# Kernel optimization log

Hardware: AMD Instinct MI355X
Metric: run time of the kernel (lower is better)

## Reference

```python
import jax, jax.numpy as jnp
import numpy as np

B, T, D = 2, 2048, 1024
N_HEADS = 16
HEAD_DIM = D // N_HEADS
HIDDEN = 4 * D
LN_EPS = 1e-6  # flax LayerNorm default


def apply_rotary_pos_emb(x, positions):
    # x: (B, T, H, head_dim); positions: (T,)
    head_dim = x.shape[-1]
    inv_freq = 1.0 / 10000 ** (jnp.arange(0, head_dim, 2).astype(jnp.float32) / head_dim)
    freqs = jnp.outer(positions.astype(jnp.float32), inv_freq)  # (T, head_dim//2)
    cos_emb = jnp.cos(freqs)[None, :, None, :]
    sin_emb = jnp.sin(freqs)[None, :, None, :]
    x1 = x[..., : head_dim // 2]
    x2 = x[..., head_dim // 2 :]
    return jnp.concatenate([x1 * cos_emb - x2 * sin_emb,
                            x1 * sin_emb + x2 * cos_emb], axis=-1)


def layernorm(x, scale, bias):
    mu = jnp.mean(x, axis=-1, keepdims=True)
    var = jnp.mean(jnp.square(x - mu), axis=-1, keepdims=True)
    return (x - mu) * jax.lax.rsqrt(var + LN_EPS) * scale + bias


def setup_inputs() -> dict:
    key = jax.random.key(0)
    ks = jax.random.split(key, 8)
    lecun = lambda k, shape: jax.random.normal(k, shape, jnp.float32) * (1.0 / np.sqrt(shape[0]))
    x = jax.random.normal(ks[0], (B, T, D), jnp.float32)
    positions = jnp.arange(T, dtype=jnp.int32)
    mask = jnp.tril(jnp.ones((T, T), dtype=bool))[None, None]  # causal (1,1,T,T)
    return {
        "x": x,
        "positions": positions,
        "mask": mask,
        "ln1_scale": jnp.ones((D,), jnp.float32),
        "ln1_bias": jnp.zeros((D,), jnp.float32),
        "w_qkv": lecun(ks[1], (D, 3 * D)),
        "w_o": lecun(ks[2], (D, D)),
        "ln2_scale": jnp.ones((D,), jnp.float32),
        "ln2_bias": jnp.zeros((D,), jnp.float32),
        "w1": lecun(ks[3], (D, HIDDEN)),
        "b1": jnp.zeros((HIDDEN,), jnp.float32),
        "w2": lecun(ks[4], (HIDDEN, D)),
        "b2": jnp.zeros((D,), jnp.float32),
    }


def reference(x, positions, mask, ln1_scale, ln1_bias, w_qkv, w_o,
              ln2_scale, ln2_bias, w1, b1, w2, b2):
    h = layernorm(x, ln1_scale, ln1_bias)
    qkv = h @ w_qkv  # (B,T,3D)
    qkv = qkv.reshape(B, T, 3, N_HEADS, HEAD_DIM)
    q, k, v = jnp.moveaxis(qkv, 2, 0)  # each (B,T,H,hd)
    q = apply_rotary_pos_emb(q, positions)
    k = apply_rotary_pos_emb(k, positions)
    q = jnp.transpose(q, (0, 2, 1, 3))  # (B,H,T,hd)
    k = jnp.transpose(k, (0, 2, 1, 3))
    v = jnp.transpose(v, (0, 2, 1, 3))
    scale = 1.0 / jnp.sqrt(jnp.float32(HEAD_DIM))
    attn_weights = jnp.einsum('bhqd,bhkd->bhqk', q, k) * scale
    attn_weights = jnp.where(mask, attn_weights, -1e10)
    attn_weights = jax.nn.softmax(attn_weights, axis=-1)
    h = jnp.einsum('bhqk,bhkd->bhqd', attn_weights, v)
    h = jnp.transpose(h, (0, 2, 1, 3)).reshape(B, T, D)
    h = h @ w_o
    x = x + h
    h = layernorm(x, ln2_scale, ln2_bias)
    h = jax.nn.gelu(h @ w1 + b1)  # approximate gelu, matching flax nn.gelu default
    h = h @ w2 + b2
    return x + h
```

## Files before the change

kernel.cpp:

```cpp
#include <hip/hip_runtime.h>


typedef __bf16 bf16_t;
typedef bf16_t bf16x8 __attribute__((ext_vector_type(8)));
typedef float f32x4 __attribute__((ext_vector_type(4)));

#define M_ROWS 4096
#define DMODEL 1024
#define TSEQ   2048
#define NHEAD  16
#define HDIM   64

__device__ __forceinline__ ushort f2bf(float f) {
  union { float f; unsigned u; } v; v.f = f;
  unsigned r = (v.u + 0x7fffu + ((v.u >> 16) & 1u)) >> 16;
  return (ushort)r;
}
__device__ __forceinline__ float bf2f(ushort u) {
  union { unsigned u; float f; } v; v.u = ((unsigned)u) << 16;
  return v.f;
}
__device__ __forceinline__ unsigned cvt_pk_bf16(float a, float b) {
  unsigned r;
  asm("v_cvt_pk_bf16_f32 %0, %1, %2" : "=v"(r) : "v"(a), "v"(b));
  return r;
}
__device__ __forceinline__ void gload_lds16(const void* g, void* l) {
  __builtin_amdgcn_global_load_lds(
      (const __attribute__((address_space(1))) unsigned*)g,
      (__attribute__((address_space(3))) unsigned*)l, 16, 0, 0);
}
__device__ __forceinline__ f32x4 mfma16(bf16x8 a, bf16x8 b, f32x4 c) {
  return __builtin_amdgcn_mfma_f32_16x16x32_bf16(a, b, c, 0, 0, 0);
}
__device__ __forceinline__ float gelu_f(float x) {
  float y = 0.7978845608028654f * (x + 0.044715f * x * x * x);
  float e = __expf(2.0f * y);
  float t = 1.0f - 2.0f / (e + 1.0f);
  return 0.5f * x * (1.0f + t);
}

__global__ __launch_bounds__(256)
void transpose_bf16(const float* __restrict__ src, ushort* __restrict__ dst,
                    int K, int N) {
  __shared__ float t[32][33];
  int n0 = blockIdx.x * 32, k0 = blockIdx.y * 32;
  int tx = threadIdx.x & 31, ty = threadIdx.x >> 5;
#pragma unroll
  for (int i = 0; i < 4; i++) {
    int k = ty + i * 8;
    t[k][tx] = src[(size_t)(k0 + k) * N + n0 + tx];
  }
  __syncthreads();
#pragma unroll
  for (int i = 0; i < 4; i++) {
    int nn = ty + i * 8;
    dst[(size_t)(n0 + nn) * K + k0 + tx] = f2bf(t[tx][nn]);
  }
}

__global__ __launch_bounds__(256)
void ln_kernel(const float* __restrict__ x, const float* __restrict__ sc,
               const float* __restrict__ bi, ushort* __restrict__ out) {
  int row = blockIdx.x;
  int tid = threadIdx.x;
  const float4 v = *(const float4*)&x[(size_t)row * DMODEL + tid * 4];
  float s = v.x + v.y + v.z + v.w;
  float s2 = v.x * v.x + v.y * v.y + v.z * v.z + v.w * v.w;
#pragma unroll
  for (int off = 32; off > 0; off >>= 1) {
    s += __shfl_down(s, off);
    s2 += __shfl_down(s2, off);
  }
  __shared__ float red[8];
  int lane = tid & 63, w = tid >> 6;
  if (lane == 0) { red[w * 2] = s; red[w * 2 + 1] = s2; }
  __syncthreads();
  float S = red[0] + red[2] + red[4] + red[6];
  float S2 = red[1] + red[3] + red[5] + red[7];
  float mu = S * (1.0f / DMODEL);
  float var = S2 * (1.0f / DMODEL) - mu * mu;
  float rs = rsqrtf(var + 1e-6f);
  float4 scv = *(const float4*)&sc[tid * 4];
  float4 biv = *(const float4*)&bi[tid * 4];
  ushort4 o;
  o.x = f2bf((v.x - mu) * rs * scv.x + biv.x);
  o.y = f2bf((v.y - mu) * rs * scv.y + biv.y);
  o.z = f2bf((v.z - mu) * rs * scv.z + biv.z);
  o.w = f2bf((v.w - mu) * rs * scv.w + biv.w);
  *(ushort4*)&out[(size_t)row * DMODEL + tid * 4] = o;
}

__global__ __launch_bounds__(256)
void rope_table(const int* __restrict__ positions, float2* __restrict__ tab) {
  int i = blockIdx.x * 256 + threadIdx.x;
  int t = i >> 5, f = i & 31;
  float inv = __expf(-(float)f * (1.0f / 32.0f) * 9.210340371976184f);
  float a = (float)positions[t] * inv;
  tab[i] = make_float2(cosf(a), sinf(a));
}

__global__ __launch_bounds__(256)
void rope_apply(const ushort* __restrict__ qkv, const float2* __restrict__ tab,
                ushort* __restrict__ Q, ushort* __restrict__ Kd,
                ushort* __restrict__ VT) {
  __shared__ ushort vt[64][66];
  int t0 = blockIdx.x * 64;
  int bh = blockIdx.y;
  int b = bh >> 4, h = bh & 15;
  int f = threadIdx.x & 31, tg = threadIdx.x >> 5;
#pragma unroll
  for (int i = 0; i < 8; i++) {
    int tt = tg * 8 + i;
    int t = t0 + tt;
    const ushort* qr = qkv + (size_t)(b * TSEQ + t) * 3072 + h * 64 + f;
    float2 cs = tab[t * 32 + f];
    float c = cs.x, s = cs.y;
    float q1 = bf2f(qr[0]),    q2 = bf2f(qr[32]);
    float k1 = bf2f(qr[1024]), k2 = bf2f(qr[1056]);
    ushort* Qp = Q + ((size_t)bh * TSEQ + t) * HDIM;
    ushort* Kp = Kd + ((size_t)bh * TSEQ + t) * HDIM;
    Qp[f]      = f2bf(q1 * c - q2 * s);
    Qp[f + 32] = f2bf(q1 * s + q2 * c);
    Kp[f]      = f2bf(k1 * c - k2 * s);
    Kp[f + 32] = f2bf(k1 * s + k2 * c);
    vt[f][tt]      = qr[2048];
    vt[f + 32][tt] = qr[2080];
  }
  __syncthreads();
  int t = threadIdx.x & 63, fg = threadIdx.x >> 6;
  ushort* Vp = VT + (size_t)bh * HDIM * TSEQ + t0 + t;
#pragma unroll
  for (int j = 0; j < 16; j++) {
    int ff = fg * 16 + j;
    Vp[(size_t)ff * TSEQ] = vt[ff][t];
  }
}

__global__ __launch_bounds__(256, 4)
void attn_kernel(const ushort* __restrict__ Q, const ushort* __restrict__ Kd,
                 const ushort* __restrict__ VT, ushort* __restrict__ O) {
  int bh = blockIdx.x;
  int p = blockIdx.y;
  int tid = threadIdx.x;
  int lane = tid & 63, w = tid >> 6;
  int lr = lane & 15, lg = lane >> 4;

  const ushort* Qb = Q + (size_t)bh * TSEQ * HDIM;
  const ushort* Kb = Kd + (size_t)bh * TSEQ * HDIM;
  const ushort* Vb = VT + (size_t)bh * HDIM * TSEQ;

  __shared__ ushort lK[2][64 * 64];
  __shared__ ushort lV[2][64 * 64];
  __shared__ ushort pt[4][16 * 64];
  ushort* myp = pt[w];

  int srow0 = tid >> 3, sch = tid & 7;

  auto stage = [&](int buf, int kt) {
#pragma unroll
    for (int c = 0; c < 2; c++) {
      int r = c * 32 + srow0;
      int gch = sch ^ (r & 7);
      gload_lds16(Kb + (size_t)(kt + r) * HDIM + gch * 8,
                  &lK[buf][c * 2048 + tid * 8]);
      gload_lds16(Vb + (size_t)r * TSEQ + kt + gch * 8,
                  &lV[buf][c * 2048 + tid * 8]);
    }
  };

  const float QS = 0.125f * 1.44269504088896340736f;
  int b = bh >> 4, h = bh & 15;

  for (int half = 0; half < 2; half++) {
    int qb = half == 0 ? (31 - p) : p;
    int nt = qb + 1;
    int qw = qb * 64 + w * 16;
    int q_abs = qw + lr;

    bf16x8 aq0 = *(const bf16x8*)&Qb[(size_t)q_abs * HDIM + lg * 8];
    bf16x8 aq1 = *(const bf16x8*)&Qb[(size_t)q_abs * HDIM + 32 + lg * 8];
#pragma unroll
    for (int j = 0; j < 8; j++) {
      aq0[j] = (bf16_t)((float)aq0[j] * QS);
      aq1[j] = (bf16_t)((float)aq1[j] * QS);
    }

    float m_run = -1e30f, l_run = 0.0f;
    f32x4 o[4] = {};

    stage(0, 0);
    __syncthreads();

    for (int it = 0; it < nt; ++it) {
      int kt = it * 64;
      int buf = it & 1;
      bool diag = (it == nt - 1);

      if (it + 1 < nt) stage(buf ^ 1, kt + 64);

      f32x4 sa[4];
#pragma unroll
      for (int cb = 0; cb < 4; cb++) {
        int row = cb * 16 + lr;
        const ushort* kp = &lK[buf][row * 64];
        bf16x8 k0 = *(const bf16x8*)(kp + (((lg    ) ^ (row & 7)) << 3));
        bf16x8 k1 = *(const bf16x8*)(kp + (((lg + 4) ^ (row & 7)) << 3));
        f32x4 z = {};
        z = mfma16(k0, aq0, z);
        sa[cb] = mfma16(k1, aq1, z);
      }

      if (diag) {
#pragma unroll
        for (int cb = 0; cb < 4; cb++)
#pragma unroll
          for (int r = 0; r < 4; r++)
            if (kt + cb * 16 + lg * 4 + r > q_abs) sa[cb][r] = -1e30f;
      }

      f32x4 m4;
#pragma unroll
      for (int r = 0; r < 4; r++)
        m4[r] = fmaxf(fmaxf(sa[0][r], sa[1][r]), fmaxf(sa[2][r], sa[3][r]));
      float mx = fmaxf(fmaxf(m4[0], m4[1]), fmaxf(m4[2], m4[3]));
      mx = fmaxf(mx, __shfl_xor(mx, 16, 64));
      mx = fmaxf(mx, __shfl_xor(mx, 32, 64));
      float mn = fmaxf(m_run, mx);
      float rescale = __builtin_amdgcn_exp2f(m_run - mn);
      m_run = mn;

      float ps = 0.0f;
      uint2 pk[4];
#pragma unroll
      for (int cb = 0; cb < 4; cb++) {
        float p0 = __builtin_amdgcn_exp2f(sa[cb][0] - mn);
        float p1 = __builtin_amdgcn_exp2f(sa[cb][1] - mn);
        float p2 = __builtin_amdgcn_exp2f(sa[cb][2] - mn);
        float p3 = __builtin_amdgcn_exp2f(sa[cb][3] - mn);
        ps += (p0 + p1) + (p2 + p3);
        pk[cb].x = cvt_pk_bf16(p0, p1);
        pk[cb].y = cvt_pk_bf16(p2, p3);
      }
      ps += __shfl_xor(ps, 16, 64);
      ps += __shfl_xor(ps, 32, 64);
      l_run = l_run * rescale + ps;

#pragma unroll
      for (int cb = 0; cb < 4; cb++)
        *(uint2*)&myp[lr * 64 + (((cb * 4 + lg) ^ lr) << 2)] = pk[cb];

#pragma unroll
      for (int d = 0; d < 4; d++)
#pragma unroll
        for (int r = 0; r < 4; r++) o[d][r] *= rescale;

      union U8 { uint2 h[2]; bf16x8 v; };
      U8 t0, t1;
      t0.h[0] = *(const uint2*)&myp[lr * 64 + (((lg * 2    ) ^ lr) << 2)];
      t0.h[1] = *(const uint2*)&myp[lr * 64 + (((lg * 2 + 1) ^ lr) << 2)];
      t1.h[0] = *(const uint2*)&myp[lr * 64 + (((8 + lg * 2    ) ^ lr) << 2)];
      t1.h[1] = *(const uint2*)&myp[lr * 64 + (((8 + lg * 2 + 1) ^ lr) << 2)];

#pragma unroll
      for (int d = 0; d < 4; d++) {
        int row = d * 16 + lr;
        const ushort* vp = &lV[buf][row * 64];
        bf16x8 va0 = *(const bf16x8*)(vp + (((lg    ) ^ (row & 7)) << 3));
        bf16x8 va1 = *(const bf16x8*)(vp + (((lg + 4) ^ (row & 7)) << 3));
        o[d] = mfma16(va0, t0.v, o[d]);
        o[d] = mfma16(va1, t1.v, o[d]);
      }

      __syncthreads();
    }

    float linv = 1.0f / l_run;
    size_t obase = (size_t)(b * TSEQ + qw + lr) * DMODEL + h * 64;
#pragma unroll
    for (int d = 0; d < 4; d++) {
      uint2 st;
      st.x = cvt_pk_bf16(o[d][0] * linv, o[d][1] * linv);
      st.y = cvt_pk_bf16(o[d][2] * linv, o[d][3] * linv);
      *(uint2*)&O[obase + d * 16 + lg * 4] = st;
    }
  }
}

template <int EPI, int BN>
__global__ __launch_bounds__(256)
void gemm_kernel(const ushort* __restrict__ A, const ushort* __restrict__ Bt,
                 void* __restrict__ Cout, const float* __restrict__ bias,
                 const float* __restrict__ resid, int M, int N, int K,
                 int nbn) {
  constexpr int NF = BN / 32;
  __shared__ ushort lA[2][128 * 64];
  __shared__ ushort lB[2][BN * 64];
  int tid = threadIdx.x;
  int lane = tid & 63, w = tid >> 6;
  int wm = w >> 1, wn = w & 1;

  int nwg = gridDim.x;
  int cpx = nwg >> 3;
  int wg = ((int)blockIdx.x & 7) * cpx + ((int)blockIdx.x >> 3);
  int bm = wg / nbn, bn = wg % nbn;

  f32x4 acc[4][NF] = {};

  const ushort* Ab = A + (size_t)bm * 128 * K;
  const ushort* Bb = Bt + (size_t)bn * BN * K;
  int lrow = lane & 15, lg = lane >> 4;
  int srow = tid >> 3, sch = tid & 7;

  auto stage = [&](int buf, int k0) {
#pragma unroll
    for (int c = 0; c < 4; c++) {
      int r = c * 32 + srow;
      int gch = sch ^ (r & 7);
      gload_lds16(Ab + (size_t)r * K + k0 + gch * 8,
                  &lA[buf][c * 2048 + tid * 8]);
    }
#pragma unroll
    for (int c = 0; c < NF; c++) {
      int r = c * 32 + srow;
      int gch = sch ^ (r & 7);
      gload_lds16(Bb + (size_t)r * K + k0 + gch * 8,
                  &lB[buf][c * 2048 + tid * 8]);
    }
  };

  int nt = K >> 6;
  stage(0, 0);
  __syncthreads();

  for (int t = 0; t < nt; ++t) {
    int cur = t & 1;

    bf16x8 af0[4], af1[4], bf0[NF], bf1[NF];
#pragma unroll
    for (int m = 0; m < 4; m++) {
      int row = wm * 64 + m * 16 + lrow;
      const ushort* p = &lA[cur][row * 64];
      af0[m] = *(const bf16x8*)(p + (((lg    ) ^ (row & 7)) << 3));
      af1[m] = *(const bf16x8*)(p + (((lg + 4) ^ (row & 7)) << 3));
    }
#pragma unroll
    for (int n = 0; n < NF; n++) {
      int row = wn * (BN / 2) + n * 16 + lrow;
      const ushort* p = &lB[cur][row * 64];
      bf0[n] = *(const bf16x8*)(p + (((lg    ) ^ (row & 7)) << 3));
      bf1[n] = *(const bf16x8*)(p + (((lg + 4) ^ (row & 7)) << 3));
    }

    if (t + 1 < nt) stage(cur ^ 1, (t + 1) << 6);

    __builtin_amdgcn_s_setprio(1);
#pragma unroll
    for (int m = 0; m < 4; m++)
#pragma unroll
      for (int n = 0; n < NF; n++)
        acc[m][n] = mfma16(af0[m], bf0[n], acc[m][n]);
#pragma unroll
    for (int m = 0; m < 4; m++)
#pragma unroll
      for (int n = 0; n < NF; n++)
        acc[m][n] = mfma16(af1[m], bf1[n], acc[m][n]);
    __builtin_amdgcn_s_setprio(0);

    __builtin_amdgcn_sched_barrier(0);
    asm volatile("s_waitcnt vmcnt(0)" ::: "memory");
    __builtin_amdgcn_s_barrier();
  }

#pragma unroll
  for (int m = 0; m < 4; m++) {
    int rbase = bm * 128 + wm * 64 + m * 16 + (lane >> 4) * 4;
#pragma unroll
    for (int n = 0; n < NF; n++) {
      int c = bn * BN + wn * (BN / 2) + n * 16 + (lane & 15);
#pragma unroll
      for (int r = 0; r < 4; r++) {
        float v = acc[m][n][r];
        size_t idx = (size_t)(rbase + r) * N + c;
        if constexpr (EPI == 0) {
          ((ushort*)Cout)[idx] = f2bf(v);
        } else if constexpr (EPI == 1) {
          ((float*)Cout)[idx] = v + resid[idx];
        } else if constexpr (EPI == 2) {
          ((ushort*)Cout)[idx] = f2bf(gelu_f(v + bias[c]));
        } else {
          ((float*)Cout)[idx] = v + bias[c] + resid[idx];
        }
      }
    }
  }
}

extern "C" void kernel_launch(void* const* d_in, const int* in_sizes, int n_in,
                              void* d_out, int out_size, void* d_ws,
                              size_t ws_size, hipStream_t stream) {
  const float* x      = (const float*)d_in[0];
  const int* positions = (const int*)d_in[1];
  const float* ln1_s  = (const float*)d_in[3];
  const float* ln1_b  = (const float*)d_in[4];
  const float* w_qkv  = (const float*)d_in[5];
  const float* w_o    = (const float*)d_in[6];
  const float* ln2_s  = (const float*)d_in[7];
  const float* ln2_b  = (const float*)d_in[8];
  const float* w1     = (const float*)d_in[9];
  const float* b1     = (const float*)d_in[10];
  const float* w2     = (const float*)d_in[11];
  const float* b2     = (const float*)d_in[12];
  float* out = (float*)d_out;

  char* ws = (char*)d_ws;
  size_t off = 0;
  auto nxt = [&](size_t bytes) {
    char* p = ws + off;
    off += (bytes + 255) & ~(size_t)255;
    return p;
  };
  ushort* wqkvT = (ushort*)nxt(3072ULL * 1024 * 2);
  ushort* woT   = (ushort*)nxt(1024ULL * 1024 * 2);
  ushort* w1T   = (ushort*)nxt(4096ULL * 1024 * 2);
  ushort* w2T   = (ushort*)nxt(1024ULL * 4096 * 2);
  ushort* h1    = (ushort*)nxt((size_t)M_ROWS * DMODEL * 2);
  ushort* qkv   = (ushort*)nxt((size_t)M_ROWS * 3072 * 2);
  ushort* Qb    = (ushort*)nxt(2ULL * NHEAD * TSEQ * HDIM * 2);
  ushort* Kb    = (ushort*)nxt(2ULL * NHEAD * TSEQ * HDIM * 2);
  ushort* VTb   = (ushort*)nxt(2ULL * NHEAD * TSEQ * HDIM * 2);
  ushort* attn  = (ushort*)nxt((size_t)M_ROWS * DMODEL * 2);
  float*  x2    = (float*)nxt((size_t)M_ROWS * DMODEL * 4);
  ushort* h2    = (ushort*)nxt((size_t)M_ROWS * DMODEL * 2);
  ushort* mid   = (ushort*)nxt((size_t)M_ROWS * 4096 * 2);
  float2* tab   = (float2*)nxt((size_t)TSEQ * 32 * 8);

  transpose_bf16<<<dim3(3072 / 32, 1024 / 32), 256, 0, stream>>>(w_qkv, wqkvT, 1024, 3072);
  transpose_bf16<<<dim3(1024 / 32, 1024 / 32), 256, 0, stream>>>(w_o, woT, 1024, 1024);
  transpose_bf16<<<dim3(4096 / 32, 1024 / 32), 256, 0, stream>>>(w1, w1T, 1024, 4096);
  transpose_bf16<<<dim3(1024 / 32, 4096 / 32), 256, 0, stream>>>(w2, w2T, 4096, 1024);
  rope_table<<<(TSEQ * 32) / 256, 256, 0, stream>>>(positions, tab);
  ln_kernel<<<M_ROWS, 256, 0, stream>>>(x, ln1_s, ln1_b, h1);
  gemm_kernel<0, 64><<<1536, 256, 0, stream>>>(h1, wqkvT, qkv, nullptr, nullptr, 4096, 3072, 1024, 48);
  rope_apply<<<dim3(TSEQ / 64, 2 * NHEAD), 256, 0, stream>>>(qkv, tab, Qb, Kb, VTb);
  attn_kernel<<<dim3(32, 16), 256, 0, stream>>>(Qb, Kb, VTb, attn);
  gemm_kernel<1, 64><<<512, 256, 0, stream>>>(attn, woT, x2, nullptr, x, 4096, 1024, 1024, 16);
  ln_kernel<<<M_ROWS, 256, 0, stream>>>(x2, ln2_s, ln2_b, h2);
  gemm_kernel<2, 128><<<1024, 256, 0, stream>>>(h2, w1T, mid, b1, nullptr, 4096, 4096, 1024, 32);
  gemm_kernel<3, 64><<<512, 256, 0, stream>>>(mid, w2T, out, b2, x2, 4096, 1024, 4096, 16);
}
```

Baseline: 230.6 us.

## Fuse RoPE, Q scaling and V transpose into QKV GEMM epilogue; merge transposes

```diff
diff --git a/kernel.cpp b/kernel.cpp
--- a/kernel.cpp
+++ b/kernel.cpp
@@ -41,10 +41,18 @@
 }
 
 __global__ __launch_bounds__(256)
-void transpose_bf16(const float* __restrict__ src, ushort* __restrict__ dst,
-                    int K, int N) {
+void transpose_all(const float* __restrict__ wqkv, const float* __restrict__ wo,
+                   const float* __restrict__ w1, const float* __restrict__ w2,
+                   ushort* __restrict__ dqkv, ushort* __restrict__ dwo,
+                   ushort* __restrict__ dw1, ushort* __restrict__ dw2) {
+  int id = blockIdx.x;
+  const float* src; ushort* dst; int K, N, nx, loc;
+  if (id < 3072)      { src = wqkv; dst = dqkv; K = 1024; N = 3072; nx = 96;  loc = id; }
+  else if (id < 4096) { src = wo;   dst = dwo;  K = 1024; N = 1024; nx = 32;  loc = id - 3072; }
+  else if (id < 8192) { src = w1;   dst = dw1;  K = 1024; N = 4096; nx = 128; loc = id - 4096; }
+  else                { src = w2;   dst = dw2;  K = 4096; N = 1024; nx = 32;  loc = id - 8192; }
+  int n0 = (loc % nx) * 32, k0 = (loc / nx) * 32;
   __shared__ float t[32][33];
-  int n0 = blockIdx.x * 32, k0 = blockIdx.y * 32;
   int tx = threadIdx.x & 31, ty = threadIdx.x >> 5;
 #pragma unroll
   for (int i = 0; i < 4; i++) {
@@ -101,39 +109,139 @@
 }
 
 __global__ __launch_bounds__(256)
-void rope_apply(const ushort* __restrict__ qkv, const float2* __restrict__ tab,
-                ushort* __restrict__ Q, ushort* __restrict__ Kd,
-                ushort* __restrict__ VT) {
-  __shared__ ushort vt[64][66];
-  int t0 = blockIdx.x * 64;
-  int bh = blockIdx.y;
-  int b = bh >> 4, h = bh & 15;
-  int f = threadIdx.x & 31, tg = threadIdx.x >> 5;
-#pragma unroll
-  for (int i = 0; i < 8; i++) {
-    int tt = tg * 8 + i;
-    int t = t0 + tt;
-    const ushort* qr = qkv + (size_t)(b * TSEQ + t) * 3072 + h * 64 + f;
-    float2 cs = tab[t * 32 + f];
-    float c = cs.x, s = cs.y;
-    float q1 = bf2f(qr[0]),    q2 = bf2f(qr[32]);
-    float k1 = bf2f(qr[1024]), k2 = bf2f(qr[1056]);
-    ushort* Qp = Q + ((size_t)bh * TSEQ + t) * HDIM;
-    ushort* Kp = Kd + ((size_t)bh * TSEQ + t) * HDIM;
-    Qp[f]      = f2bf(q1 * c - q2 * s);
-    Qp[f + 32] = f2bf(q1 * s + q2 * c);
-    Kp[f]      = f2bf(k1 * c - k2 * s);
-    Kp[f + 32] = f2bf(k1 * s + k2 * c);
-    vt[f][tt]      = qr[2048];
-    vt[f + 32][tt] = qr[2080];
-  }
+void qkv_gemm(const ushort* __restrict__ A, const ushort* __restrict__ Bt,
+              const float2* __restrict__ tab, ushort* __restrict__ Qo,
+              ushort* __restrict__ Ko, ushort* __restrict__ VTo, int K,
+              int nbn) {
+  constexpr int NF = 2;
+  __shared__ char smem[49152];
+  ushort* lA = (ushort*)smem;
+  ushort* lB = (ushort*)(smem + 32768);
+  int tid = threadIdx.x;
+  int lane = tid & 63, w = tid >> 6;
+  int wm = w >> 1, wn = w & 1;
+
+  int nwg = gridDim.x;
+  int cpx = nwg >> 3;
+  int wg = ((int)blockIdx.x & 7) * cpx + ((int)blockIdx.x >> 3);
+  int bm = wg / nbn, bn = wg % nbn;
+
+  f32x4 acc[4][NF] = {};
+
+  const ushort* Ab = A + (size_t)bm * 128 * K;
+  const ushort* Bb = Bt + (size_t)bn * 64 * K;
+  int lrow = lane & 15, lg = lane >> 4;
+  int srow = tid >> 3, sch = tid & 7;
+
+  auto stage = [&](int buf, int k0) {
+#pragma unroll
+    for (int c = 0; c < 4; c++) {
+      int r = c * 32 + srow;
+      int gch = sch ^ (r & 7);
+      gload_lds16(Ab + (size_t)r * K + k0 + gch * 8,
+                  &lA[buf * 8192 + c * 2048 + tid * 8]);
+    }
+#pragma unroll
+    for (int c = 0; c < 2; c++) {
+      int r = c * 32 + srow;
+      int gch = sch ^ (r & 7);
+      gload_lds16(Bb + (size_t)r * K + k0 + gch * 8,
+                  &lB[buf * 4096 + c * 2048 + tid * 8]);
+    }
+  };
+
+  int nt = K >> 6;
+  stage(0, 0);
   __syncthreads();
-  int t = threadIdx.x & 63, fg = threadIdx.x >> 6;
-  ushort* Vp = VT + (size_t)bh * HDIM * TSEQ + t0 + t;
-#pragma unroll
-  for (int j = 0; j < 16; j++) {
-    int ff = fg * 16 + j;
-    Vp[(size_t)ff * TSEQ] = vt[ff][t];
+
+  for (int t = 0; t < nt; ++t) {
+    int cur = t & 1;
+    bf16x8 af0[4], af1[4], bf0[NF], bf1[NF];
+#pragma unroll
+    for (int m = 0; m < 4; m++) {
+      int row = wm * 64 + m * 16 + lrow;
+      const ushort* p = &lA[cur * 8192 + row * 64];
+      af0[m] = *(const bf16x8*)(p + (((lg    ) ^ (row & 7)) << 3));
+      af1[m] = *(const bf16x8*)(p + (((lg + 4) ^ (row & 7)) << 3));
+    }
+#pragma unroll
+    for (int n = 0; n < NF; n++) {
+      int row = wn * 32 + n * 16 + lrow;
+      const ushort* p = &lB[cur * 4096 + row * 64];
+      bf0[n] = *(const bf16x8*)(p + (((lg    ) ^ (row & 7)) << 3));
+      bf1[n] = *(const bf16x8*)(p + (((lg + 4) ^ (row & 7)) << 3));
+    }
+    if (t + 1 < nt) stage(cur ^ 1, (t + 1) << 6);
+    __builtin_amdgcn_s_setprio(1);
+#pragma unroll
+    for (int m = 0; m < 4; m++)
+#pragma unroll
+      for (int n = 0; n < NF; n++)
+        acc[m][n] = mfma16(af0[m], bf0[n], acc[m][n]);
+#pragma unroll
+    for (int m = 0; m < 4; m++)
+#pragma unroll
+      for (int n = 0; n < NF; n++)
+        acc[m][n] = mfma16(af1[m], bf1[n], acc[m][n]);
+    __builtin_amdgcn_s_setprio(0);
+    __builtin_amdgcn_sched_barrier(0);
+    asm volatile("s_waitcnt vmcnt(0)" ::: "memory");
+    __builtin_amdgcn_s_barrier();
+  }
+
+  float* lt = (float*)smem;
+#pragma unroll
+  for (int m = 0; m < 4; m++) {
+    int row = wm * 64 + m * 16 + lg * 4;
+#pragma unroll
+    for (int n = 0; n < NF; n++) {
+      int col = wn * 32 + n * 16 + lrow;
+#pragma unroll
+      for (int r = 0; r < 4; r++)
+        lt[(row + r) * 68 + col] = acc[m][n][r];
+    }
+  }
+  __syncthreads();
+
+  int t0 = bm * 128;
+  int b = t0 >> 11;
+  int tloc = t0 & 2047;
+
+  if (bn < 32) {
+    bool isQ = (bn < 16);
+    int h = bn & 15;
+    const float QS = 0.125f * 1.44269504088896340736f;
+    float sc = isQ ? QS : 1.0f;
+    ushort* dst = (isQ ? Qo : Ko) + ((size_t)(b * NHEAD + h) * TSEQ) * HDIM;
+    int row = tid >> 1, f0 = (tid & 1) * 16;
+    int t = tloc + row;
+    ushort lo[16], hi[16];
+#pragma unroll
+    for (int j = 0; j < 16; j++) {
+      int f = f0 + j;
+      float2 cs = tab[t * 32 + f];
+      float x1 = lt[row * 68 + f], x2 = lt[row * 68 + f + 32];
+      lo[j] = f2bf((x1 * cs.x - x2 * cs.y) * sc);
+      hi[j] = f2bf((x1 * cs.y + x2 * cs.x) * sc);
+    }
+    ushort* dr = dst + (size_t)t * HDIM;
+#pragma unroll
+    for (int c = 0; c < 4; c++) {
+      *(ushort4*)&dr[f0 + c * 4]      = *(ushort4*)&lo[c * 4];
+      *(ushort4*)&dr[32 + f0 + c * 4] = *(ushort4*)&hi[c * 4];
+    }
+  } else {
+    int h = bn - 32;
+    ushort* dst = VTo + (size_t)(b * NHEAD + h) * HDIM * TSEQ;
+    int f = tid >> 2, tc0 = (tid & 3) * 32;
+    ushort buf[32];
+#pragma unroll
+    for (int j = 0; j < 32; j++)
+      buf[j] = f2bf(lt[(tc0 + j) * 68 + f]);
+    ushort* dr = dst + (size_t)f * TSEQ + tloc + tc0;
+#pragma unroll
+    for (int c = 0; c < 8; c++)
+      *(ushort4*)&dr[c * 4] = *(ushort4*)&buf[c * 4];
   }
 }
 
@@ -169,7 +277,6 @@
     }
   };
 
-  const float QS = 0.125f * 1.44269504088896340736f;
   int b = bh >> 4, h = bh & 15;
 
   for (int half = 0; half < 2; half++) {
@@ -180,11 +287,6 @@
 
     bf16x8 aq0 = *(const bf16x8*)&Qb[(size_t)q_abs * HDIM + lg * 8];
     bf16x8 aq1 = *(const bf16x8*)&Qb[(size_t)q_abs * HDIM + 32 + lg * 8];
-#pragma unroll
-    for (int j = 0; j < 8; j++) {
-      aq0[j] = (bf16_t)((float)aq0[j] * QS);
-      aq1[j] = (bf16_t)((float)aq1[j] * QS);
-    }
 
     float m_run = -1e30f, l_run = 0.0f;
     f32x4 o[4] = {};
@@ -425,7 +527,6 @@
   ushort* w1T   = (ushort*)nxt(4096ULL * 1024 * 2);
   ushort* w2T   = (ushort*)nxt(1024ULL * 4096 * 2);
   ushort* h1    = (ushort*)nxt((size_t)M_ROWS * DMODEL * 2);
-  ushort* qkv   = (ushort*)nxt((size_t)M_ROWS * 3072 * 2);
   ushort* Qb    = (ushort*)nxt(2ULL * NHEAD * TSEQ * HDIM * 2);
   ushort* Kb    = (ushort*)nxt(2ULL * NHEAD * TSEQ * HDIM * 2);
   ushort* VTb   = (ushort*)nxt(2ULL * NHEAD * TSEQ * HDIM * 2);
@@ -435,14 +536,11 @@
   ushort* mid   = (ushort*)nxt((size_t)M_ROWS * 4096 * 2);
   float2* tab   = (float2*)nxt((size_t)TSEQ * 32 * 8);
 
-  transpose_bf16<<<dim3(3072 / 32, 1024 / 32), 256, 0, stream>>>(w_qkv, wqkvT, 1024, 3072);
-  transpose_bf16<<<dim3(1024 / 32, 1024 / 32), 256, 0, stream>>>(w_o, woT, 1024, 1024);
-  transpose_bf16<<<dim3(4096 / 32, 1024 / 32), 256, 0, stream>>>(w1, w1T, 1024, 4096);
-  transpose_bf16<<<dim3(1024 / 32, 4096 / 32), 256, 0, stream>>>(w2, w2T, 4096, 1024);
+  transpose_all<<<12288, 256, 0, stream>>>(w_qkv, w_o, w1, w2,
+                                           wqkvT, woT, w1T, w2T);
   rope_table<<<(TSEQ * 32) / 256, 256, 0, stream>>>(positions, tab);
   ln_kernel<<<M_ROWS, 256, 0, stream>>>(x, ln1_s, ln1_b, h1);
-  gemm_kernel<0, 64><<<1536, 256, 0, stream>>>(h1, wqkvT, qkv, nullptr, nullptr, 4096, 3072, 1024, 48);
-  rope_apply<<<dim3(TSEQ / 64, 2 * NHEAD), 256, 0, stream>>>(qkv, tab, Qb, Kb, VTb);
+  qkv_gemm<<<1536, 256, 0, stream>>>(h1, wqkvT, tab, Qb, Kb, VTb, 1024, 48);
   attn_kernel<<<dim3(32, 16), 256, 0, stream>>>(Qb, Kb, VTb, attn);
   gemm_kernel<1, 64><<<512, 256, 0, stream>>>(attn, woT, x2, nullptr, x, 4096, 1024, 1024, 16);
   ln_kernel<<<M_ROWS, 256, 0, stream>>>(x2, ln2_s, ln2_b, h2);
```

After: 225.9 us. 2.0% less time.
